# Performance work log

Measured on AMD Instinct MI355X. Metric: run time of the kernel, lower is better.

The kernel has to match this reference:

```python
import jax, jax.numpy as jnp
import numpy as np

N_NODES = 10000
N_EDGES = 320000
N_GRAPHS = 64
L = 3  # num_layers


def _gru(a, h, wih, whh, bih, bhh):
    # torch.nn.GRUCell math: input a, hidden h
    gi = a @ wih.T + bih
    gh = h @ whh.T + bhh
    ir, iz, inn = jnp.split(gi, 3, axis=-1)
    hr, hz, hn = jnp.split(gh, 3, axis=-1)
    r = jax.nn.sigmoid(ir + hr)
    z = jax.nn.sigmoid(iz + hz)
    n = jnp.tanh(inn + r * hn)
    return (1.0 - z) * n + z * h


def _ggc(x, src, dst, w, wih, whh, bih, bhh):
    # PyG GatedGraphConv: pad features up to out_channels, then L rounds of
    # (linear -> scatter-add over edges -> GRUCell update)
    out_ch = w.shape[-1]
    if x.shape[-1] < out_ch:
        x = jnp.concatenate(
            [x, jnp.zeros((x.shape[0], out_ch - x.shape[-1]), x.dtype)], axis=-1)
    for i in range(w.shape[0]):
        m = x @ w[i]                                        # [N, C]
        a = jax.ops.segment_sum(m[src], dst, num_segments=N_NODES)  # scatter-add
        x = _gru(a, x, wih, whh, bih, bhh)
    return x


def setup_inputs() -> dict:
    key = jax.random.key(0)
    ks = jax.random.split(key, 16)
    d1, d2 = 128, 256
    s1, s2 = 1.0 / np.sqrt(d1), 1.0 / np.sqrt(d2)
    x = jax.random.normal(ks[0], (N_NODES, d1), dtype=jnp.float32)
    edge_index = jax.random.randint(ks[1], (2, N_EDGES), 0, N_NODES, dtype=jnp.int64)
    batch = jnp.sort(jax.random.randint(ks[2], (N_NODES,), 0, N_GRAPHS, dtype=jnp.int64))
    return {
        "x": x,
        "edge_index": edge_index,
        "batch": batch,
        "w1": jax.random.normal(ks[3], (L, d1, d1), jnp.float32) * s1,
        "gru1_wih": jax.random.normal(ks[4], (3 * d1, d1), jnp.float32) * s1,
        "gru1_whh": jax.random.normal(ks[5], (3 * d1, d1), jnp.float32) * s1,
        "gru1_bih": jax.random.normal(ks[6], (3 * d1,), jnp.float32) * s1,
        "gru1_bhh": jax.random.normal(ks[7], (3 * d1,), jnp.float32) * s1,
        "w2": jax.random.normal(ks[8], (L, d2, d2), jnp.float32) * s2,
        "gru2_wih": jax.random.normal(ks[9], (3 * d2, d2), jnp.float32) * s2,
        "gru2_whh": jax.random.normal(ks[10], (3 * d2, d2), jnp.float32) * s2,
        "gru2_bih": jax.random.normal(ks[11], (3 * d2,), jnp.float32) * s2,
        "gru2_bhh": jax.random.normal(ks[12], (3 * d2,), jnp.float32) * s2,
        "fc_w": jax.random.normal(ks[13], (6, d2), jnp.float32) * s2,
        "fc_b": jnp.zeros((6,), jnp.float32),
    }


def reference(x, edge_index, batch, w1, gru1_wih, gru1_whh, gru1_bih, gru1_bhh,
              w2, gru2_wih, gru2_whh, gru2_bih, gru2_bhh, fc_w, fc_b):
    src, dst = edge_index[0], edge_index[1]
    y = jax.nn.relu(_ggc(x, src, dst, w1, gru1_wih, gru1_whh, gru1_bih, gru1_bhh))
    y = _ggc(y, src, dst, w2, gru2_wih, gru2_whh, gru2_bih, gru2_bhh)
    y = jax.ops.segment_max(y, batch, num_segments=N_GRAPHS)  # global max pool [G, 256]
    return y @ fc_w.T + fc_b  # [G, 6]
```

## Files before the change

### kernel.cpp

```cpp
#include <hip/hip_runtime.h>

#define NN 10000
#define NNP 10112
#define NE 320000
#define NG 64
#define D1 128
#define D2 256
#define MT 158

typedef unsigned short u16;
typedef short v8s __attribute__((ext_vector_type(8)));
typedef float v4f __attribute__((ext_vector_type(4)));

__device__ __forceinline__ u16 f2bf(float x) {
    unsigned u = __float_as_uint(x);
    return (u16)((u + 0x7fffu + ((u >> 16) & 1u)) >> 16);
}
__device__ __forceinline__ float bf2f(u16 b) {
    return __uint_as_float(((unsigned)b) << 16);
}
__device__ __forceinline__ float sigm(float x) { return 1.f / (1.f + __expf(-x)); }
__device__ __forceinline__ float tanh_f(float x) {
    float cx = fminf(fmaxf(x, -15.f), 15.f);
    float e = __expf(2.f * cx);
    return (e - 1.f) / (e + 1.f);
}

#define MF(d, a, b) d = __builtin_amdgcn_mfma_f32_16x16x32_bf16(a, b, d, 0, 0, 0)

#define SWZ(bx, by)                              \
    const int bid_ = blockIdx.x;                 \
    const int l_ = bid_ >> 3;                    \
    const int by = (bid_ & 7) * 20 + l_ % 20;    \
    const int bx = l_ / 20;                      \
    if (by >= MT) return;


template<int MODE, int OS>
__global__ __launch_bounds__(256, 3)
void giqru_k(const u16* __restrict__ Ah, const u16* __restrict__ Al,
             const u16* __restrict__ Xh, const u16* __restrict__ Xl,
             const u16* __restrict__ WcH, const u16* __restrict__ WcL,
             const float* __restrict__ bih, const float* __restrict__ bhh,
             u16* __restrict__ xh_out, u16* __restrict__ xl_out,
             float* __restrict__ xf_out,
             const int* __restrict__ batch, unsigned* __restrict__ pool,
             int C) {
    SWZ(bx, by)
    const int tid = threadIdx.x;
    const int wave = tid >> 6, lane = tid & 63;
    const int wm = (wave >> 1) * 32, wn = (wave & 1) * 64;
    const int bm = by * 64, bn = bx * 128;
    const int quad = lane >> 4, r16 = lane & 15;
    const int K2 = 2 * C;
    const int NK = K2 >> 5;
    const int CCH = C >> 3;
    const size_t arow = (size_t)(bm >> 6) * CCH;
    const size_t wrow = (size_t)(bn >> 7) * (K2 >> 3);
    const int aoff0 = (wm + r16) * 8;
    const int woff0 = (wn + r16) * 8;

    auto LOAD = [&](int ks, v8s* fah, v8s* fal, v8s* wh, v8s* wl) {
        const int k0 = ks << 5;
        const bool ap = k0 < C;
        const u16* sh = ap ? Ah : Xh;
        const u16* sl = ap ? Al : Xl;
        const int kk = ap ? k0 : k0 - C;
        const size_t ach = (arow + (kk >> 3) + quad) * 512;
        const size_t wch = (wrow + (k0 >> 3) + quad) * 1024;
        const int g2 = ap ? 2 : 3;
#pragma unroll
        for (int i = 0; i < 2; ++i) {
            fah[i] = *(const v8s*)(sh + ach + aoff0 + i * 128);
            fal[i] = *(const v8s*)(sl + ach + aoff0 + i * 128);
        }
        wh[0] = *(const v8s*)(WcH + wch + woff0);
        wl[0] = *(const v8s*)(WcL + wch + woff0);
        wh[1] = *(const v8s*)(WcH + wch + woff0 + 128);
        wl[1] = *(const v8s*)(WcL + wch + woff0 + 128);
        wh[2] = *(const v8s*)(WcH + wch + woff0 + g2 * 128);
        wl[2] = *(const v8s*)(WcL + wch + woff0 + g2 * 128);
    };

    v4f acc[2][4] = {};
    auto STEP = [&](v8s* fah, v8s* fal, v8s* wh, v8s* wl, bool ap) {
#pragma unroll
        for (int i = 0; i < 2; ++i) {
            MF(acc[i][0], fah[i], wh[0]); MF(acc[i][0], fah[i], wl[0]); MF(acc[i][0], fal[i], wh[0]);
            MF(acc[i][1], fah[i], wh[1]); MF(acc[i][1], fah[i], wl[1]); MF(acc[i][1], fal[i], wh[1]);
            if (ap) {
                MF(acc[i][2], fah[i], wh[2]); MF(acc[i][2], fah[i], wl[2]); MF(acc[i][2], fal[i], wh[2]);
            } else {
                MF(acc[i][3], fah[i], wh[2]); MF(acc[i][3], fah[i], wl[2]); MF(acc[i][3], fal[i], wh[2]);
            }
        }
    };

    v8s ahA[2], alA[2], whA[3], wlA[3];
    v8s ahB[2], alB[2], whB[3], wlB[3];
    LOAD(0, ahA, alA, whA, wlA);
    for (int ks = 0; ks < NK; ks += 2) {
        LOAD(ks + 1, ahB, alB, whB, wlB);
        STEP(ahA, alA, whA, wlA, (ks << 5) < C);
        if (ks + 2 < NK) LOAD(ks + 2, ahA, alA, whA, wlA);
        STEP(ahB, alB, whB, wlB, ((ks + 1) << 5) < C);
    }

    const int c = bx * 32 + (wn ? 16 : 0) + r16;
    const float br = bih[c] + bhh[c];
    const float bz = bih[C + c] + bhh[C + c];
    const float bi_n = bih[2 * C + c];
    const float bh_n = bhh[2 * C + c];
    const int cch = c >> 3, cr = c & 7;
#pragma unroll
    for (int i = 0; i < 2; ++i) {
        int R0 = bm + wm + i * 16 + quad * 4;
#pragma unroll
        for (int r = 0; r < 4; ++r) {
            int R = R0 + r;
            if (R >= NN) continue;
            float rr = sigm(acc[i][0][r] + br);
            float zz = sigm(acc[i][1][r] + bz);
            float nn_ = tanh_f(acc[i][2][r] + bi_n + rr * (acc[i][3][r] + bh_n));
            size_t hx = ((size_t)(R >> 6) * CCH + cch) * 512 + ((R & 63) << 3) + cr;
            float h = bf2f(Xh[hx]) + bf2f(Xl[hx]);
            float o = (1.f - zz) * nn_ + zz * h;
            if (MODE == 2) {
                unsigned b = __float_as_uint(o);
                unsigned u = (b & 0x80000000u) ? ~b : (b | 0x80000000u);
                atomicMax(&pool[batch[R] * 256 + c], u);
            } else {
                if (MODE == 1) o = fmaxf(o, 0.f);
                size_t ox = ((size_t)(R >> 6) * (OS >> 3) + cch) * 512 + ((R & 63) << 3) + cr;
                u16 hh = f2bf(o);
                xh_out[ox] = hh;
                xl_out[ox] = f2bf(o - bf2f(hh));
                xf_out[(size_t)R * OS + c] = o;
            }
        }
    }
}

__global__ void count_k(const int* __restrict__ dst, int* __restrict__ cnt) {
    int e = blockIdx.x * blockDim.x + threadIdx.x;
    if (e < NE) atomicAdd(&cnt[dst[e]], 1);
}

__global__ void scan_k(const int* __restrict__ cnt, int* __restrict__ off,
                       int* __restrict__ cur) {
    __shared__ int ps[1024];
    const int tid = threadIdx.x;
    const int CH = (NN + 1023) / 1024;
    const int base = tid * CH;
    int s = 0;
    for (int i = 0; i < CH; ++i) {
        int idx = base + i;
        if (idx < NN) s += cnt[idx];
    }
    ps[tid] = s;
    __syncthreads();
    for (int d = 1; d < 1024; d <<= 1) {
        int v = (tid >= d) ? ps[tid - d] : 0;
        __syncthreads();
        ps[tid] += v;
        __syncthreads();
    }
    int run = (tid > 0) ? ps[tid - 1] : 0;
    for (int i = 0; i < CH; ++i) {
        int idx = base + i;
        if (idx <= NN) { off[idx] = run; if (idx < NN) cur[idx] = run; }
        if (idx < NN) run += cnt[idx];
    }
}

__global__ void fill_k(const int* __restrict__ src, const int* __restrict__ dst,
                       int* __restrict__ cur, int* __restrict__ elist) {
    int e = blockIdx.x * blockDim.x + threadIdx.x;
    if (e >= NE) return;
    int p = atomicAdd(&cur[dst[e]], 1);
    elist[p] = src[e];
}

template<int C>
__global__ void gather_k(const float* __restrict__ xf, const int* __restrict__ off,
                         const int* __restrict__ elist,
                         u16* __restrict__ ah, u16* __restrict__ al) {
    constexpr int LPN = C / 4;
    const int GB = gridDim.x;
    const int q = GB >> 3, r = GB & 7;
    const int xx = blockIdx.x & 7, oo = blockIdx.x >> 3;
    const int wg = (xx < r ? xx * (q + 1) : r * (q + 1) + (xx - r) * q) + oo;
    int t = wg * 256 + threadIdx.x;
    int node = t / LPN;
    if (node >= NN) return;
    int c = (t % LPN) * 4;
    int s0 = off[node], s1 = off[node + 1];
    v4f a0 = 0.f, a1 = 0.f, a2 = 0.f, a3 = 0.f;
    int i = s0;
    for (; i + 4 <= s1; i += 4) {
        int e0 = elist[i], e1 = elist[i + 1], e2 = elist[i + 2], e3 = elist[i + 3];
        v4f v0 = *(const v4f*)(xf + (size_t)e0 * C + c);
        v4f v1 = *(const v4f*)(xf + (size_t)e1 * C + c);
        v4f v2 = *(const v4f*)(xf + (size_t)e2 * C + c);
        v4f v3 = *(const v4f*)(xf + (size_t)e3 * C + c);
        a0 += v0; a1 += v1; a2 += v2; a3 += v3;
    }
    for (; i < s1; ++i) {
        int e = elist[i];
        a0 += *(const v4f*)(xf + (size_t)e * C + c);
    }
    v4f acc = (a0 + a1) + (a2 + a3);
    ushort4 h, l;
    h.x = f2bf(acc[0]); l.x = f2bf(acc[0] - bf2f(h.x));
    h.y = f2bf(acc[1]); l.y = f2bf(acc[1] - bf2f(h.y));
    h.z = f2bf(acc[2]); l.z = f2bf(acc[2] - bf2f(h.z));
    h.w = f2bf(acc[3]); l.w = f2bf(acc[3] - bf2f(h.w));
    size_t ox = ((size_t)(node >> 6) * (C >> 3) + (c >> 3)) * 512 + ((node & 63) << 3) + (c & 7);
    *(ushort4*)(ah + ox) = h;
    *(ushort4*)(al + ox) = l;
}

__global__ void weff_k(const float* __restrict__ w, const float* __restrict__ wih,
                       u16* __restrict__ WcH, u16* __restrict__ WcL, int C) {
    __shared__ float As[64 * 65];
    __shared__ float Bs[64 * 65];
    const int k0 = blockIdx.x * 64, jp0 = blockIdx.y * 64, it = blockIdx.z;
    const int tid = threadIdx.x;
    const int tx = tid & 15, ty = tid >> 4;
    const int K2 = 2 * C;
    float acc[4][4] = {};
    for (int j0 = 0; j0 < C; j0 += 64) {
        for (int idx = tid; idx < 4096; idx += 256) {
            int row = idx >> 6, j = idx & 63;
            As[row * 65 + j] = w[((size_t)it * C + k0 + row) * C + j0 + j];
            int jp = jp0 + row;
            int cc = ((jp >> 6) << 4) | (jp & 15);
            int g = (jp >> 4) & 3;
            Bs[row * 65 + j] = (g < 3) ? wih[((size_t)g * C + cc) * C + j0 + j] : 0.f;
        }
        __syncthreads();
        for (int j = 0; j < 64; ++j) {
            float a0 = As[(tx * 4 + 0) * 65 + j];
            float a1 = As[(tx * 4 + 1) * 65 + j];
            float a2 = As[(tx * 4 + 2) * 65 + j];
            float a3 = As[(tx * 4 + 3) * 65 + j];
            float b0 = Bs[(ty * 4 + 0) * 65 + j];
            float b1 = Bs[(ty * 4 + 1) * 65 + j];
            float b2 = Bs[(ty * 4 + 2) * 65 + j];
            float b3 = Bs[(ty * 4 + 3) * 65 + j];
            acc[0][0] += b0 * a0; acc[0][1] += b0 * a1; acc[0][2] += b0 * a2; acc[0][3] += b0 * a3;
            acc[1][0] += b1 * a0; acc[1][1] += b1 * a1; acc[1][2] += b1 * a2; acc[1][3] += b1 * a3;
            acc[2][0] += b2 * a0; acc[2][1] += b2 * a1; acc[2][2] += b2 * a2; acc[2][3] += b2 * a3;
            acc[3][0] += b3 * a0; acc[3][1] += b3 * a1; acc[3][2] += b3 * a2; acc[3][3] += b3 * a3;
        }
        __syncthreads();
    }
    const size_t its = (size_t)it * 8 * C * C;
#pragma unroll
    for (int a = 0; a < 4; ++a) {
        int jp = jp0 + ty * 4 + a;
#pragma unroll
        for (int b = 0; b < 4; ++b) {
            int k = k0 + tx * 4 + b;
            float v = acc[a][b];
            u16 h = f2bf(v);
            size_t o = its + ((size_t)(jp >> 7) * (K2 >> 3) + (k >> 3)) * 1024 + ((jp & 127) << 3) + (k & 7);
            WcH[o] = h;
            WcL[o] = f2bf(v - bf2f(h));
        }
    }
}

__global__ void prep_k(const float* __restrict__ whh1, const float* __restrict__ whh2,
                       const float* __restrict__ xin,
                       u16* __restrict__ Wc1h, u16* __restrict__ Wc1l,
                       u16* __restrict__ Wc2h, u16* __restrict__ Wc2l,
                       u16* __restrict__ xh, u16* __restrict__ xl) {
    const int q1 = 3 * 512 * 128;
    const int q2 = 3 * 1024 * 256;
    int t = blockIdx.x * blockDim.x + threadIdx.x;
    if (t < q1) {
        int it = t / (512 * 128), r = t - it * (512 * 128);
        int jp = r >> 7, kk = r & 127;
        int c = ((jp >> 6) << 4) | (jp & 15);
        int g = (jp >> 4) & 3;
        float v = (g == 0) ? whh1[c * D1 + kk]
                : (g == 1) ? whh1[(D1 + c) * D1 + kk]
                : (g == 2) ? 0.f
                           : whh1[(2 * D1 + c) * D1 + kk];
        int k = D1 + kk;
        u16 h = f2bf(v);
        size_t o = (size_t)it * 131072 + ((size_t)(jp >> 7) * 32 + (k >> 3)) * 1024 + ((jp & 127) << 3) + (k & 7);
        Wc1h[o] = h; Wc1l[o] = f2bf(v - bf2f(h)); return;
    }
    t -= q1;
    if (t < q2) {
        int it = t / (1024 * 256), r = t - it * (1024 * 256);
        int jp = r >> 8, kk = r & 255;
        int c = ((jp >> 6) << 4) | (jp & 15);
        int g = (jp >> 4) & 3;
        float v = (g == 0) ? whh2[c * D2 + kk]
                : (g == 1) ? whh2[(D2 + c) * D2 + kk]
                : (g == 2) ? 0.f
                           : whh2[(2 * D2 + c) * D2 + kk];
        int k = D2 + kk;
        u16 h = f2bf(v);
        size_t o = (size_t)it * 524288 + ((size_t)(jp >> 7) * 64 + (k >> 3)) * 1024 + ((jp & 127) << 3) + (k & 7);
        Wc2h[o] = h; Wc2l[o] = f2bf(v - bf2f(h)); return;
    }
    t -= q2;
    if (t < NN * D1) {
        int n = t >> 7, cc = t & 127;
        float v = xin[t];
        u16 h = f2bf(v);
        size_t o = ((size_t)(n >> 6) * 16 + (cc >> 3)) * 512 + ((n & 63) << 3) + (cc & 7);
        xh[o] = h;
        xl[o] = f2bf(v - bf2f(h));
    }
}

__global__ void pad_k(u16* __restrict__ xh, u16* __restrict__ xl,
                      float* __restrict__ xf) {
    int t = blockIdx.x * blockDim.x + threadIdx.x;
    if (t >= NNP * 128) return;
    int n = t >> 7, c = 128 + (t & 127);
    size_t o = ((size_t)(n >> 6) * 32 + (c >> 3)) * 512 + ((n & 63) << 3) + (c & 7);
    xh[o] = 0;
    xl[o] = 0;
    xf[(size_t)n * 256 + c] = 0.f;
}

__global__ void pool_init_k(unsigned* __restrict__ pool) {
    int t = blockIdx.x * blockDim.x + threadIdx.x;
    if (t < NG * D2) pool[t] = 0x007FFFFFu;
}

__global__ void fc_k(const unsigned* __restrict__ pool, const float* __restrict__ w,
                     const float* __restrict__ b, float* __restrict__ out) {
    int t = blockIdx.x * blockDim.x + threadIdx.x;
    if (t >= NG * 6) return;
    int g = t / 6, o = t - g * 6;
    float s = b[o];
    for (int c = 0; c < D2; ++c) {
        unsigned u = pool[g * D2 + c];
        unsigned bits = (u & 0x80000000u) ? (u ^ 0x80000000u) : ~u;
        s += __uint_as_float(bits) * w[o * D2 + c];
    }
    out[t] = s;
}

extern "C" void kernel_launch(void* const* d_in, const int* in_sizes, int n_in,
                              void* d_out, int out_size, void* d_ws, size_t ws_size,
                              hipStream_t stream) {
    const float* x_in = (const float*)d_in[0];
    const int* ei = (const int*)d_in[1];
    const int* src = ei;
    const int* dst = ei + NE;
    const int* batch = (const int*)d_in[2];
    const float* w1   = (const float*)d_in[3];
    const float* wih1 = (const float*)d_in[4];
    const float* whh1 = (const float*)d_in[5];
    const float* bih1 = (const float*)d_in[6];
    const float* bhh1 = (const float*)d_in[7];
    const float* w2   = (const float*)d_in[8];
    const float* wih2 = (const float*)d_in[9];
    const float* whh2 = (const float*)d_in[10];
    const float* bih2 = (const float*)d_in[11];
    const float* bhh2 = (const float*)d_in[12];
    const float* fcw  = (const float*)d_in[13];
    const float* fcb  = (const float*)d_in[14];
    float* out = (float*)d_out;

    u16* a_h  = (u16*)d_ws;
    u16* a_l  = a_h + (size_t)NNP * 256;
    u16* xA0h = a_l + (size_t)NNP * 256;
    u16* xA0l = xA0h + (size_t)NNP * 128;
    u16* xA1h = xA0l + (size_t)NNP * 128;
    u16* xA1l = xA1h + (size_t)NNP * 128;
    u16* xB0h = xA1l + (size_t)NNP * 128;
    u16* xB0l = xB0h + (size_t)NNP * 256;
    u16* xB1h = xB0l + (size_t)NNP * 256;
    u16* xB1l = xB1h + (size_t)NNP * 256;
    u16* Wc1h = xB1l + (size_t)NNP * 256;
    u16* Wc1l = Wc1h + (size_t)3 * 512 * 256;
    u16* Wc2h = Wc1l + (size_t)3 * 512 * 256;
    u16* Wc2l = Wc2h + (size_t)3 * 1024 * 512;
    float* xfA = (float*)(Wc2l + (size_t)3 * 1024 * 512);
    float* xfB = xfA + (size_t)NNP * 128;
    int* cnt   = (int*)(xfB + (size_t)NNP * 256);
    int* off   = cnt + NN;
    int* cur   = off + NN + 1;
    int* elist = cur + NN;
    unsigned* pool = (unsigned*)(elist + NE);

    hipMemsetAsync(cnt, 0, NN * sizeof(int), stream);
    count_k<<<(NE + 255) / 256, 256, 0, stream>>>(dst, cnt);
    scan_k<<<1, 1024, 0, stream>>>(cnt, off, cur);
    fill_k<<<(NE + 255) / 256, 256, 0, stream>>>(src, dst, cur, elist);
    {
        int total = 3 * 512 * 128 + 3 * 1024 * 256 + NN * D1;
        prep_k<<<(total + 255) / 256, 256, 0, stream>>>(
            whh1, whh2, x_in, Wc1h, Wc1l, Wc2h, Wc2l, xA0h, xA0l);
    }
    weff_k<<<dim3(D1 / 64, 4 * D1 / 64, 3), 256, 0, stream>>>(w1, wih1, Wc1h, Wc1l, D1);
    weff_k<<<dim3(D2 / 64, 4 * D2 / 64, 3), 256, 0, stream>>>(w2, wih2, Wc2h, Wc2l, D2);
    pad_k<<<(NNP * 128 + 255) / 256, 256, 0, stream>>>(xB0h, xB0l, xfB);
    pool_init_k<<<(NG * D2 + 255) / 256, 256, 0, stream>>>(pool);

    const int G1 = 160 * 4;
    const int G2 = 160 * 8;
    const int GG1 = (NN * (D1 / 4) + 255) / 256;
    const int GG2 = (NN * (D2 / 4) + 255) / 256;
    const size_t W1S = 131072, W2S = 524288;

    gather_k<D1><<<GG1, 256, 0, stream>>>(x_in, off, elist, a_h, a_l);
    giqru_k<0, 128><<<G1, 256, 0, stream>>>(
        a_h, a_l, xA0h, xA0l, Wc1h, Wc1l, bih1, bhh1,
        xA1h, xA1l, xfA, nullptr, nullptr, D1);

    gather_k<D1><<<GG1, 256, 0, stream>>>(xfA, off, elist, a_h, a_l);
    giqru_k<0, 128><<<G1, 256, 0, stream>>>(
        a_h, a_l, xA1h, xA1l, Wc1h + W1S, Wc1l + W1S, bih1, bhh1,
        xA0h, xA0l, xfA, nullptr, nullptr, D1);

    gather_k<D1><<<GG1, 256, 0, stream>>>(xfA, off, elist, a_h, a_l);
    giqru_k<1, 256><<<G1, 256, 0, stream>>>(
        a_h, a_l, xA0h, xA0l, Wc1h + 2 * W1S, Wc1l + 2 * W1S, bih1, bhh1,
        xB0h, xB0l, xfB, nullptr, nullptr, D1);

    gather_k<D2><<<GG2, 256, 0, stream>>>(xfB, off, elist, a_h, a_l);
    giqru_k<0, 256><<<G2, 256, 0, stream>>>(
        a_h, a_l, xB0h, xB0l, Wc2h, Wc2l, bih2, bhh2,
        xB1h, xB1l, xfB, nullptr, nullptr, D2);

    gather_k<D2><<<GG2, 256, 0, stream>>>(xfB, off, elist, a_h, a_l);
    giqru_k<0, 256><<<G2, 256, 0, stream>>>(
        a_h, a_l, xB1h, xB1l, Wc2h + W2S, Wc2l + W2S, bih2, bhh2,
        xB0h, xB0l, xfB, nullptr, nullptr, D2);

    gather_k<D2><<<GG2, 256, 0, stream>>>(xfB, off, elist, a_h, a_l);
    giqru_k<2, 256><<<G2, 256, 0, stream>>>(
        a_h, a_l, xB0h, xB0l, Wc2h + 2 * W2S, Wc2l + 2 * W2S, bih2, bhh2,
        nullptr, nullptr, nullptr, batch, pool, D2);

    fc_k<<<1, 512, 0, stream>>>(pool, fcw, fcb, out);
}
```

Before: 576.7 us.

## Retile fused GRU GEMM so each wave covers all 64 rows with compile-time C

The fused aggregate+GRU GEMM kernel now assigns each wave all 64 rows of the block and one 16-column output group, instead of a 32x32 quarter. This doubles the columns per block and halves the grid. C becomes a template parameter so the K loop can be fully unrolled, and the manual A/B double-buffered prefetch is replaced by a straight unrolled loop. Launch bounds drop to 2 blocks per SM to make room for the larger accumulator array. The intent is fewer redundant A-fragment reloads per weight fragment, traded against fewer waves and reliance on the compiler to schedule loads ahead of the MFMAs.

```diff
diff --git a/kernel.cpp b/kernel.cpp
--- a/kernel.cpp
+++ b/kernel.cpp
@@ -36,56 +36,53 @@
     if (by >= MT) return;
 
 
-template<int MODE, int OS>
-__global__ __launch_bounds__(256, 3)
+template<int C, int MODE, int OS>
+__global__ __launch_bounds__(256, 2)
 void giqru_k(const u16* __restrict__ Ah, const u16* __restrict__ Al,
              const u16* __restrict__ Xh, const u16* __restrict__ Xl,
              const u16* __restrict__ WcH, const u16* __restrict__ WcL,
              const float* __restrict__ bih, const float* __restrict__ bhh,
              u16* __restrict__ xh_out, u16* __restrict__ xl_out,
              float* __restrict__ xf_out,
-             const int* __restrict__ batch, unsigned* __restrict__ pool,
-             int C) {
+             const int* __restrict__ batch, unsigned* __restrict__ pool) {
     SWZ(bx, by)
     const int tid = threadIdx.x;
     const int wave = tid >> 6, lane = tid & 63;
-    const int wm = (wave >> 1) * 32, wn = (wave & 1) * 64;
-    const int bm = by * 64, bn = bx * 128;
+    const int bm = by * 64;
     const int quad = lane >> 4, r16 = lane & 15;
-    const int K2 = 2 * C;
-    const int NK = K2 >> 5;
-    const int CCH = C >> 3;
-    const size_t arow = (size_t)(bm >> 6) * CCH;
-    const size_t wrow = (size_t)(bn >> 7) * (K2 >> 3);
-    const int aoff0 = (wm + r16) * 8;
-    const int woff0 = (wn + r16) * 8;
-
-    auto LOAD = [&](int ks, v8s* fah, v8s* fal, v8s* wh, v8s* wl) {
+    constexpr int K2 = 2 * C;
+    constexpr int NK = K2 >> 5;
+    constexpr int CCH = C >> 3;
+    const size_t arow = (size_t)by * CCH;
+    const size_t wtile = (size_t)(bx * 2 + (wave >> 1)) * (K2 >> 3);
+    const int aoff = r16 * 8;
+    const int woff = ((wave & 1) * 64 + r16) * 8;
+
+    v4f acc[4][4] = {};
+#pragma unroll
+    for (int ks = 0; ks < NK; ++ks) {
         const int k0 = ks << 5;
         const bool ap = k0 < C;
+        const int kk = ap ? k0 : k0 - C;
         const u16* sh = ap ? Ah : Xh;
         const u16* sl = ap ? Al : Xl;
-        const int kk = ap ? k0 : k0 - C;
         const size_t ach = (arow + (kk >> 3) + quad) * 512;
-        const size_t wch = (wrow + (k0 >> 3) + quad) * 1024;
+        const size_t wch = (wtile + (k0 >> 3) + quad) * 1024;
         const int g2 = ap ? 2 : 3;
-#pragma unroll
-        for (int i = 0; i < 2; ++i) {
-            fah[i] = *(const v8s*)(sh + ach + aoff0 + i * 128);
-            fal[i] = *(const v8s*)(sl + ach + aoff0 + i * 128);
-        }
-        wh[0] = *(const v8s*)(WcH + wch + woff0);
-        wl[0] = *(const v8s*)(WcL + wch + woff0);
-        wh[1] = *(const v8s*)(WcH + wch + woff0 + 128);
-        wl[1] = *(const v8s*)(WcL + wch + woff0 + 128);
-        wh[2] = *(const v8s*)(WcH + wch + woff0 + g2 * 128);
-        wl[2] = *(const v8s*)(WcL + wch + woff0 + g2 * 128);
-    };
-
-    v4f acc[2][4] = {};
-    auto STEP = [&](v8s* fah, v8s* fal, v8s* wh, v8s* wl, bool ap) {
-#pragma unroll
-        for (int i = 0; i < 2; ++i) {
+        v8s fah[4], fal[4], wh[3], wl[3];
+#pragma unroll
+        for (int i = 0; i < 4; ++i) {
+            fah[i] = *(const v8s*)(Ah + 0, sh + ach + aoff + i * 128);
+            fal[i] = *(const v8s*)(sl + ach + aoff + i * 128);
+        }
+        wh[0] = *(const v8s*)(WcH + wch + woff);
+        wl[0] = *(const v8s*)(WcL + wch + woff);
+        wh[1] = *(const v8s*)(WcH + wch + woff + 128);
+        wl[1] = *(const v8s*)(WcL + wch + woff + 128);
+        wh[2] = *(const v8s*)(WcH + wch + woff + g2 * 128);
+        wl[2] = *(const v8s*)(WcL + wch + woff + g2 * 128);
+#pragma unroll
+        for (int i = 0; i < 4; ++i) {
             MF(acc[i][0], fah[i], wh[0]); MF(acc[i][0], fah[i], wl[0]); MF(acc[i][0], fal[i], wh[0]);
             MF(acc[i][1], fah[i], wh[1]); MF(acc[i][1], fah[i], wl[1]); MF(acc[i][1], fal[i], wh[1]);
             if (ap) {
@@ -94,27 +91,17 @@
                 MF(acc[i][3], fah[i], wh[2]); MF(acc[i][3], fah[i], wl[2]); MF(acc[i][3], fal[i], wh[2]);
             }
         }
-    };
-
-    v8s ahA[2], alA[2], whA[3], wlA[3];
-    v8s ahB[2], alB[2], whB[3], wlB[3];
-    LOAD(0, ahA, alA, whA, wlA);
-    for (int ks = 0; ks < NK; ks += 2) {
-        LOAD(ks + 1, ahB, alB, whB, wlB);
-        STEP(ahA, alA, whA, wlA, (ks << 5) < C);
-        if (ks + 2 < NK) LOAD(ks + 2, ahA, alA, whA, wlA);
-        STEP(ahB, alB, whB, wlB, ((ks + 1) << 5) < C);
-    }
-
-    const int c = bx * 32 + (wn ? 16 : 0) + r16;
+    }
+
+    const int c = (bx * 4 + wave) * 16 + r16;
     const float br = bih[c] + bhh[c];
     const float bz = bih[C + c] + bhh[C + c];
     const float bi_n = bih[2 * C + c];
     const float bh_n = bhh[2 * C + c];
     const int cch = c >> 3, cr = c & 7;
 #pragma unroll
-    for (int i = 0; i < 2; ++i) {
-        int R0 = bm + wm + i * 16 + quad * 4;
+    for (int i = 0; i < 4; ++i) {
+        int R0 = bm + i * 16 + quad * 4;
 #pragma unroll
         for (int r = 0; r < 4; ++r) {
             int R = R0 + r;
@@ -407,41 +394,41 @@
     pad_k<<<(NNP * 128 + 255) / 256, 256, 0, stream>>>(xB0h, xB0l, xfB);
     pool_init_k<<<(NG * D2 + 255) / 256, 256, 0, stream>>>(pool);
 
-    const int G1 = 160 * 4;
-    const int G2 = 160 * 8;
+    const int G1 = 160 * 2;
+    const int G2 = 160 * 4;
     const int GG1 = (NN * (D1 / 4) + 255) / 256;
     const int GG2 = (NN * (D2 / 4) + 255) / 256;
     const size_t W1S = 131072, W2S = 524288;
 
     gather_k<D1><<<GG1, 256, 0, stream>>>(x_in, off, elist, a_h, a_l);
-    giqru_k<0, 128><<<G1, 256, 0, stream>>>(
+    giqru_k<D1, 0, 128><<<G1, 256, 0, stream>>>(
         a_h, a_l, xA0h, xA0l, Wc1h, Wc1l, bih1, bhh1,
-        xA1h, xA1l, xfA, nullptr, nullptr, D1);
+        xA1h, xA1l, xfA, nullptr, nullptr);
 
     gather_k<D1><<<GG1, 256, 0, stream>>>(xfA, off, elist, a_h, a_l);
-    giqru_k<0, 128><<<G1, 256, 0, stream>>>(
+    giqru_k<D1, 0, 128><<<G1, 256, 0, stream>>>(
         a_h, a_l, xA1h, xA1l, Wc1h + W1S, Wc1l + W1S, bih1, bhh1,
-        xA0h, xA0l, xfA, nullptr, nullptr, D1);
+        xA0h, xA0l, xfA, nullptr, nullptr);
 
     gather_k<D1><<<GG1, 256, 0, stream>>>(xfA, off, elist, a_h, a_l);
-    giqru_k<1, 256><<<G1, 256, 0, stream>>>(
+    giqru_k<D1, 1, 256><<<G1, 256, 0, stream>>>(
         a_h, a_l, xA0h, xA0l, Wc1h + 2 * W1S, Wc1l + 2 * W1S, bih1, bhh1,
-        xB0h, xB0l, xfB, nullptr, nullptr, D1);
+        xB0h, xB0l, xfB, nullptr, nullptr);
 
     gather_k<D2><<<GG2, 256, 0, stream>>>(xfB, off, elist, a_h, a_l);
-    giqru_k<0, 256><<<G2, 256, 0, stream>>>(
+    giqru_k<D2, 0, 256><<<G2, 256, 0, stream>>>(
         a_h, a_l, xB0h, xB0l, Wc2h, Wc2l, bih2, bhh2,
-        xB1h, xB1l, xfB, nullptr, nullptr, D2);
+        xB1h, xB1l, xfB, nullptr, nullptr);
 
     gather_k<D2><<<GG2, 256, 0, stream>>>(xfB, off, elist, a_h, a_l);
-    giqru_k<0, 256><<<G2, 256, 0, stream>>>(
+    giqru_k<D2, 0, 256><<<G2, 256, 0, stream>>>(
         a_h, a_l, xB1h, xB1l, Wc2h + W2S, Wc2l + W2S, bih2, bhh2,
-        xB0h, xB0l, xfB, nullptr, nullptr, D2);
+        xB0h, xB0l, xfB, nullptr, nullptr);
 
     gather_k<D2><<<GG2, 256, 0, stream>>>(xfB, off, elist, a_h, a_l);
-    giqru_k<2, 256><<<G2, 256, 0, stream>>>(
+    giqru_k<D2, 2, 256><<<G2, 256, 0, stream>>>(
         a_h, a_l, xB0h, xB0l, Wc2h + 2 * W2S, Wc2l + 2 * W2S, bih2, bhh2,
-        nullptr, nullptr, nullptr, batch, pool, D2);
+        nullptr, nullptr, nullptr, batch, pool);
 
     fc_k<<<1, 512, 0, stream>>>(pool, fcw, fcb, out);
 }
```

New measurement: 584.8 us. About the same (+1.4%).
